# Optimization experiments

Hardware: AMD Instinct MI355X
Metric: run time of the kernel (lower is better)

Reference implementation:

```python
import math
import jax, jax.numpy as jnp
import numpy as np

HEADS = 8
D_MODEL = 256


def positional_encoding_2d(c, h, w):
    # faithful port of wzlxjtu/PositionalEncoding2D
    d = c // 2
    div_term = jnp.exp(jnp.arange(0.0, d, 2, dtype=jnp.float32) * (-(math.log(10000.0) / d)))  # [d//2? no: d/2 entries -> d//2]
    pos_w = jnp.arange(0.0, w, dtype=jnp.float32)[:, None] * div_term  # [w, d//2]
    pos_h = jnp.arange(0.0, h, dtype=jnp.float32)[:, None] * div_term  # [h, d//2]
    pe = jnp.zeros((c, h, w), dtype=jnp.float32)
    sw = jnp.broadcast_to(jnp.sin(pos_w).T[:, None, :], (div_term.shape[0], h, w))
    cw = jnp.broadcast_to(jnp.cos(pos_w).T[:, None, :], (div_term.shape[0], h, w))
    sh = jnp.broadcast_to(jnp.sin(pos_h).T[:, :, None], (div_term.shape[0], h, w))
    ch = jnp.broadcast_to(jnp.cos(pos_h).T[:, :, None], (div_term.shape[0], h, w))
    pe = pe.at[0:d:2].set(sw)
    pe = pe.at[1:d:2].set(cw)
    pe = pe.at[d::2].set(sh)
    pe = pe.at[d + 1::2].set(ch)
    return pe


def setup_inputs() -> dict:
    key = jax.random.key(0)
    ks = jax.random.split(key, 9)
    b, c, h, w = 2, D_MODEL, 64, 64
    x = jax.random.normal(ks[0], (b, c, h, w), dtype=jnp.float32)
    s = 0.02
    Wq = jax.random.normal(ks[1], (c, c), dtype=jnp.float32) * s
    Wk = jax.random.normal(ks[2], (c, c), dtype=jnp.float32) * s
    Wv = jax.random.normal(ks[3], (c, c), dtype=jnp.float32) * s
    Wo = jax.random.normal(ks[4], (c, c), dtype=jnp.float32) * s
    bq = jax.random.normal(ks[5], (c,), dtype=jnp.float32) * s
    bk = jax.random.normal(ks[6], (c,), dtype=jnp.float32) * s
    bv = jax.random.normal(ks[7], (c,), dtype=jnp.float32) * s
    bo = jax.random.normal(ks[8], (c,), dtype=jnp.float32) * s
    return {"x": x, "Wq": Wq, "bq": bq, "Wk": Wk, "bk": bk,
            "Wv": Wv, "bv": bv, "Wo": Wo, "bo": bo}


def reference(x, Wq, bq, Wk, bk, Wv, bv, Wo, bo):
    b, c, h, w = x.shape
    dk = c // HEADS
    pe = positional_encoding_2d(c, h, w)
    x2 = x + pe[None]                                   # [b,c,h,w]
    tok = x2.reshape(b, c, h * w).transpose(0, 2, 1)    # [b,N,c]
    q = (tok @ Wq.T + bq).reshape(b, -1, HEADS, dk).transpose(0, 2, 1, 3)  # [b,H,N,dk]
    k = (tok @ Wk.T + bk).reshape(b, -1, HEADS, dk).transpose(0, 2, 1, 3)
    v = (tok @ Wv.T + bv).reshape(b, -1, HEADS, dk).transpose(0, 2, 1, 3)
    scores = jnp.einsum('bhnd,bhmd->bhnm', q, k) / math.sqrt(dk)  # [b,H,N,N]
    attn = jax.nn.softmax(scores, axis=-1)
    out = jnp.einsum('bhnm,bhmd->bhnd', attn, v)        # [b,H,N,dk]
    concat = out.transpose(0, 2, 1, 3).reshape(b, -1, c)  # [b,N,c]
    proj = concat @ Wo.T + bo                           # [b,N,c]
    return proj.transpose(0, 2, 1).reshape(b, c, h, w)
```

## Files before the change

kernel.cpp:

```cpp
#include <hip/hip_runtime.h>
#include <hip/hip_bf16.h>
#include <cstdint>

typedef float f32x4 __attribute__((ext_vector_type(4)));
typedef __bf16 bf16x8 __attribute__((ext_vector_type(8)));
typedef __bf16 bf16x2 __attribute__((ext_vector_type(2)));
typedef uint32_t uint2v __attribute__((ext_vector_type(2)));

#define MFMA_K32(A, B, C) __builtin_amdgcn_mfma_f32_16x16x32_bf16((A), (B), (C), 0, 0, 0)

#if __has_builtin(__builtin_amdgcn_exp2f)
#define EXP2(x) __builtin_amdgcn_exp2f(x)
#else
#define EXP2(x) exp2f(x)
#endif

static __device__ __forceinline__ uint16_t f2b(float f) {
    uint32_t u = __float_as_uint(f);
    uint32_t r = (u + 0x7fffu + ((u >> 16) & 1u)) >> 16;
    return (uint16_t)r;
}

static __device__ __forceinline__ uint32_t packbf(float a, float b) {
#if __has_builtin(__builtin_amdgcn_cvt_pk_bf16_f32)
    bf16x2 v = __builtin_amdgcn_cvt_pk_bf16_f32(a, b);
    return *(uint32_t*)&v;
#else
    uint32_t ua = __float_as_uint(a);
    ua += 0x7fffu + ((ua >> 16) & 1u);
    uint32_t ub = __float_as_uint(b);
    ub += 0x7fffu + ((ub >> 16) & 1u);
    return __builtin_amdgcn_perm(ub, ua, 0x07060302);
#endif
}

__global__ __launch_bounds__(256) void wconv_pe(const float* __restrict__ wq,
                                                const float* __restrict__ wk,
                                                const float* __restrict__ wv,
                                                const float* __restrict__ wo,
                                                uint16_t* __restrict__ dst,
                                                float* __restrict__ pet) {
    int bid = blockIdx.x, t = threadIdx.x;
    if (bid < 1024) {
        int idx = bid * 256 + t;
        int which = idx >> 16, off = idx & 65535;
        const float* s = (which == 0) ? wq : (which == 1) ? wk : (which == 2) ? wv : wo;
        dst[idx] = f2b(s[off]);
    } else {
        int idx = (bid - 1024) * 256 + t;
        int cc = idx >> 6, p = idx & 63;
        int i = (cc & 127) >> 1;
        float dt = __expf((float)(2 * i) * -0.07195578415606394f);
        float sv, cv;
        __sincosf((float)p * dt, &sv, &cv);
        pet[idx] = (cc & 1) ? cv : sv;
    }
}

__global__ __launch_bounds__(256) void peadd(const float* __restrict__ x,
                                             const float* __restrict__ pet,
                                             uint16_t* __restrict__ tok) {
    __shared__ uint16_t T[64][65];
    int t = threadIdx.x, bid = blockIdx.x;
    int nt = bid & 63, ct = (bid >> 6) & 3, bb = bid >> 8;
    int n0 = nt << 6, c0 = ct << 6;
    int nl = t & 63, cq = t >> 6;
    int n = n0 + nl;
    int posh = n0 >> 6;
#pragma unroll
    for (int p = 0; p < 16; ++p) {
        int cl = cq * 16 + p;
        int cc = c0 + cl;
        float pe = pet[cc * 64 + ((cc & 128) ? posh : nl)];
        T[cl][nl] = f2b(x[((size_t)(bb * 256 + cc) << 12) + n] + pe);
    }
    __syncthreads();
#pragma unroll
    for (int p = 0; p < 16; ++p) {
        int tl = cq * 16 + p;
        tok[(((size_t)(bb << 12) | (n0 + tl)) << 8) + c0 + nl] = T[nl][tl];
    }
}

__global__ __launch_bounds__(256) void qkv_gemm(const uint16_t* __restrict__ tok,
                                                const uint16_t* __restrict__ Wall,
                                                const float* __restrict__ bq,
                                                const float* __restrict__ bk,
                                                const float* __restrict__ bv,
                                                uint16_t* __restrict__ qo,
                                                uint16_t* __restrict__ ko,
                                                uint16_t* __restrict__ vo) {
    __shared__ __align__(16) uint16_t WS[64][264];
    int tid = threadIdx.x, wv = tid >> 6, lane = tid & 63;
    int c16 = lane & 15, quad = lane >> 4;
    int M0 = blockIdx.x * 64 + wv * 16;
    int O0 = blockIdx.y * 64;
    const uint16_t* arow = tok + (size_t)(M0 + c16) * 256;
    bf16x8 af[8];
#pragma unroll
    for (int kk = 0; kk < 8; ++kk) af[kk] = *(const bf16x8*)(arow + kk * 32 + quad * 8);
    f32x4 zero = {0.f, 0.f, 0.f, 0.f};
    int bb = M0 >> 12, n = (M0 + c16) & 4095;
    int srow = tid >> 5, sch = (tid & 31) << 3;
    for (int mat = 0; mat < 3; ++mat) {
        const uint16_t* Wg = Wall + (size_t)mat * 65536 + (size_t)O0 * 256;
        __syncthreads();
#pragma unroll
        for (int p = 0; p < 8; ++p)
            *(bf16x8*)(&WS[p * 8 + srow][sch]) = *(const bf16x8*)(Wg + (p * 8 + srow) * 256 + sch);
        __syncthreads();
        f32x4 acc[4] = {zero, zero, zero, zero};
#pragma unroll
        for (int kk = 0; kk < 8; ++kk) {
            int k0 = kk * 32 + quad * 8;
#pragma unroll
            for (int nb = 0; nb < 4; ++nb)
                acc[nb] = MFMA_K32(*(const bf16x8*)(&WS[nb * 16 + c16][k0]),
                                   af[kk], acc[nb]);
        }
        const float* bias = (mat == 0) ? bq : (mat == 1) ? bk : bv;
        if (mat < 2) {
            float scale = (mat == 0) ? 0.25505654134660127f : 1.0f;
            uint16_t* dst = (mat == 0) ? qo : ko;
#pragma unroll
            for (int nb = 0; nb < 4; ++nb) {
                int o = O0 + nb * 16 + quad * 4;
                f32x4 bi = *(const f32x4*)(bias + o);
                int h = o >> 5, dd = o & 31;
                uint2v pk;
                pk[0] = packbf((acc[nb][0] + bi[0]) * scale, (acc[nb][1] + bi[1]) * scale);
                pk[1] = packbf((acc[nb][2] + bi[2]) * scale, (acc[nb][3] + bi[3]) * scale);
                *(uint2v*)(dst + ((size_t)(bb * 8 + h) * 4096 + n) * 32 + dd) = pk;
            }
        } else {
#pragma unroll
            for (int nb = 0; nb < 4; ++nb)
#pragma unroll
                for (int r = 0; r < 4; ++r) {
                    int o = O0 + nb * 16 + quad * 4 + r;
                    vo[((size_t)(bb * 8 + (o >> 5)) * 32 + (o & 31)) * 4096 + n] =
                        f2b(acc[nb][r] + bias[o]);
                }
        }
    }
}

static __device__ __forceinline__ void attn_qblock(const bf16x8 (&kf)[4],
                                                   const bf16x8 (&vA)[2],
                                                   const bf16x8 (&vB)[2],
                                                   bf16x8 ones, bf16x8 qf,
                                                   f32x4& oA, f32x4& oB, f32x4& oS) {
    f32x4 zero = {0.f, 0.f, 0.f, 0.f};
    f32x4 s[4];
#pragma unroll
    for (int c = 0; c < 4; ++c) s[c] = MFMA_K32(kf[c], qf, zero);
#pragma unroll
    for (int p = 0; p < 2; ++p) {
#pragma unroll
        for (int r = 0; r < 4; ++r) {
            s[2 * p][r] = EXP2(s[2 * p][r]);
            s[2 * p + 1][r] = EXP2(s[2 * p + 1][r]);
        }
        union { bf16x8 v; uint32_t u[4]; } pa;
        pa.u[0] = packbf(s[2 * p][0], s[2 * p][1]);
        pa.u[1] = packbf(s[2 * p][2], s[2 * p][3]);
        pa.u[2] = packbf(s[2 * p + 1][0], s[2 * p + 1][1]);
        pa.u[3] = packbf(s[2 * p + 1][2], s[2 * p + 1][3]);
        oA = MFMA_K32(pa.v, vA[p], oA);
        oB = MFMA_K32(pa.v, vB[p], oB);
        oS = MFMA_K32(pa.v, ones, oS);
    }
}

__global__ __launch_bounds__(512, 4) void flash(const uint16_t* __restrict__ qb,
                                                const uint16_t* __restrict__ kb,
                                                const uint16_t* __restrict__ vtb,
                                                uint16_t* __restrict__ concat) {
    __shared__ __align__(16) char smem[43008];
    int tid = threadIdx.x, wv = tid >> 6, lane = tid & 63;
    int c16 = lane & 15, quad = lane >> 4;
    int half = tid >> 8, t2 = tid & 255;
    int bh = blockIdx.y;
    int q0 = (blockIdx.x << 7) + (wv & 3) * 32;
    size_t base = (size_t)bh << 12;

    uint16_t* KT = (uint16_t*)(smem + half * 21504);
    uint16_t* VT = (uint16_t*)(smem + half * 21504 + 12288);

    const uint16_t* kgp = kb + (base + (size_t)half * 2048 + (t2 >> 2)) * 32 + (t2 & 3) * 8;
    const uint16_t* vgp = vtb + ((size_t)bh * 32 + (t2 >> 3)) * 4096 + half * 2048 + (t2 & 7) * 8;
    uint16_t* kls = KT + (t2 >> 2) * 48 + (t2 & 3) * 8;
    uint16_t* vls = VT + (t2 >> 3) * 72 + (t2 & 7) * 8;

    bf16x8 qf0 = *(const bf16x8*)(qb + (base + q0 + c16) * 32 + quad * 8);
    bf16x8 qf1 = *(const bf16x8*)(qb + (base + q0 + 16 + c16) * 32 + quad * 8);

    int rbase = ((c16 >> 2) << 3) + (c16 & 3);

    union { uint32_t u[4]; bf16x8 v; } onesu;
    onesu.u[0] = 0x3F803F80u; onesu.u[1] = 0x3F803F80u;
    onesu.u[2] = 0x3F803F80u; onesu.u[3] = 0x3F803F80u;
    bf16x8 ones = onesu.v;

    f32x4 zero = {0.f, 0.f, 0.f, 0.f};
    f32x4 o00 = zero, o01 = zero, o10 = zero, o11 = zero;
    f32x4 oS0 = zero, oS1 = zero;

    {
        bf16x8 kr = *(const bf16x8*)kgp;
        bf16x8 vr = *(const bf16x8*)vgp;
        *(bf16x8*)kls = kr;
        *(bf16x8*)vls = vr;
    }
    __syncthreads();

    for (int kt = 0; kt < 32; ++kt) {
        int cur = kt & 1;
        int kn = (kt + 1) & 31;
        bf16x8 kr = *(const bf16x8*)(kgp + (size_t)kn * 2048);
        bf16x8 vr = *(const bf16x8*)(vgp + kn * 64);
        const uint16_t* kfp = KT + cur * 3072 + rbase * 48 + quad * 8;
        const uint16_t* vfp = VT + cur * 2304 + c16 * 72 + quad * 8;
        bf16x8 kf[4], vA[2], vB[2];
        kf[0] = *(const bf16x8*)(kfp);
        kf[1] = *(const bf16x8*)(kfp + 192);
        kf[2] = *(const bf16x8*)(kfp + 1536);
        kf[3] = *(const bf16x8*)(kfp + 1536 + 192);
        vA[0] = *(const bf16x8*)(vfp);
        vA[1] = *(const bf16x8*)(vfp + 32);
        vB[0] = *(const bf16x8*)(vfp + 1152);
        vB[1] = *(const bf16x8*)(vfp + 1152 + 32);
        attn_qblock(kf, vA, vB, ones, qf0, o00, o01, oS0);
        attn_qblock(kf, vA, vB, ones, qf1, o10, o11, oS1);
        *(bf16x8*)(kls + (cur ^ 1) * 3072) = kr;
        *(bf16x8*)(vls + (cur ^ 1) * 2304) = vr;
        __syncthreads();
    }

    float* ov = (float*)smem;
    if (wv >= 4) {
        float* d = ov + ((wv - 4) * 64 + lane) * 25;
#pragma unroll
        for (int r = 0; r < 4; ++r) {
            d[r] = o00[r]; d[4 + r] = o01[r]; d[8 + r] = o10[r]; d[12 + r] = o11[r];
            d[16 + r] = oS0[r]; d[20 + r] = oS1[r];
        }
    }
    __syncthreads();
    if (wv < 4) {
        const float* s = ov + (wv * 64 + lane) * 25;
#pragma unroll
        for (int r = 0; r < 4; ++r) {
            o00[r] += s[r]; o01[r] += s[4 + r]; o10[r] += s[8 + r]; o11[r] += s[12 + r];
            oS0[r] += s[16 + r]; oS1[r] += s[20 + r];
        }
        int h = bh & 7, bb = bh >> 3;
#pragma unroll
        for (int r = 0; r < 4; ++r) {
            float i0 = 1.f / oS0[r];
            float i1 = 1.f / oS1[r];
            int n = q0 + quad * 4 + r;
            size_t row0 = ((size_t)bb * 4096 + n) * 256 + h * 32;
            size_t row1 = ((size_t)bb * 4096 + n + 16) * 256 + h * 32;
            concat[row0 + c16]      = f2b(o00[r] * i0);
            concat[row0 + 16 + c16] = f2b(o01[r] * i0);
            concat[row1 + c16]      = f2b(o10[r] * i1);
            concat[row1 + 16 + c16] = f2b(o11[r] * i1);
        }
    }
}

__global__ __launch_bounds__(256) void proj_gemm(const uint16_t* __restrict__ concat,
                                                 const uint16_t* __restrict__ Wo,
                                                 const float* __restrict__ bo,
                                                 float* __restrict__ out) {
    __shared__ __align__(16) uint16_t WS[64][264];
    int tid = threadIdx.x, wv = tid >> 6, lane = tid & 63;
    int c16 = lane & 15, quad = lane >> 4;
    int M0 = blockIdx.x * 64 + wv * 16;
    int O0 = blockIdx.y * 64;
    int srow = tid >> 5, sch = (tid & 31) << 3;
    const uint16_t* Wg = Wo + (size_t)O0 * 256;
#pragma unroll
    for (int p = 0; p < 8; ++p)
        *(bf16x8*)(&WS[p * 8 + srow][sch]) = *(const bf16x8*)(Wg + (p * 8 + srow) * 256 + sch);
    const uint16_t* crow = concat + (size_t)(M0 + c16) * 256;
    bf16x8 af[8];
#pragma unroll
    for (int kk = 0; kk < 8; ++kk) af[kk] = *(const bf16x8*)(crow + kk * 32 + quad * 8);
    __syncthreads();
    f32x4 zero = {0.f, 0.f, 0.f, 0.f};
    f32x4 acc[4] = {zero, zero, zero, zero};
#pragma unroll
    for (int kk = 0; kk < 8; ++kk) {
        int k0 = kk * 32 + quad * 8;
#pragma unroll
        for (int nb = 0; nb < 4; ++nb)
            acc[nb] = MFMA_K32(*(const bf16x8*)(&WS[nb * 16 + c16][k0]),
                               af[kk], acc[nb]);
    }
    int bb = M0 >> 12, n = (M0 + c16) & 4095;
#pragma unroll
    for (int nb = 0; nb < 4; ++nb)
#pragma unroll
        for (int r = 0; r < 4; ++r) {
            int o = O0 + nb * 16 + quad * 4 + r;
            out[((size_t)(bb * 256 + o) << 12) + n] = acc[nb][r] + bo[o];
        }
}

extern "C" void kernel_launch(void* const* d_in, const int* in_sizes, int n_in,
                              void* d_out, int out_size, void* d_ws, size_t ws_size,
                              hipStream_t stream) {
    const float* x  = (const float*)d_in[0];
    const float* Wq = (const float*)d_in[1];
    const float* bq = (const float*)d_in[2];
    const float* Wk = (const float*)d_in[3];
    const float* bk = (const float*)d_in[4];
    const float* Wv = (const float*)d_in[5];
    const float* bv = (const float*)d_in[6];
    const float* Wo = (const float*)d_in[7];
    const float* bo = (const float*)d_in[8];
    float* out = (float*)d_out;

    uint16_t* ws   = (uint16_t*)d_ws;
    uint16_t* Wb   = ws;
    uint16_t* tok  = Wb + 4 * 65536;
    uint16_t* q    = tok + 2097152;
    uint16_t* k    = q + 2097152;
    uint16_t* vt   = k + 2097152;
    uint16_t* cc   = vt + 2097152;
    float*    pet  = (float*)(cc + 2097152);

    wconv_pe<<<1088, 256, 0, stream>>>(Wq, Wk, Wv, Wo, Wb, pet);
    peadd<<<512, 256, 0, stream>>>(x, pet, tok);
    qkv_gemm<<<dim3(128, 4), 256, 0, stream>>>(tok, Wb, bq, bk, bv, q, k, vt);
    flash<<<dim3(32, 16), 512, 0, stream>>>(q, k, vt, cc);
    proj_gemm<<<dim3(128, 4), 256, 0, stream>>>(cc, Wb + 3 * 65536, bo, out);
}
```

Before: 150.3 us.

## Fuse weight conversion and PE into consumers, shrink K smem padding, interleave attention blocks

Removes the separate weight-conversion and positional-encoding kernel. Weights are now converted from fp32 to bf16 while being staged into shared memory inside the QKV and projection GEMMs, and the positional encoding is computed inline in peadd with sincos. In the flash kernel the K tile row stride drops from 48 to 40, which reduces shared memory per block. The two query sub-block computations are also interleaved so their MFMA and exp chains can overlap. The cost is that each GEMM block re-reads and re-converts fp32 weights, and peadd redoes transcendental math per element.

```diff
diff --git a/kernel.cpp b/kernel.cpp
--- a/kernel.cpp
+++ b/kernel.cpp
@@ -6,6 +6,7 @@
 typedef __bf16 bf16x8 __attribute__((ext_vector_type(8)));
 typedef __bf16 bf16x2 __attribute__((ext_vector_type(2)));
 typedef uint32_t uint2v __attribute__((ext_vector_type(2)));
+typedef uint32_t uint4v __attribute__((ext_vector_type(4)));
 
 #define MFMA_K32(A, B, C) __builtin_amdgcn_mfma_f32_16x16x32_bf16((A), (B), (C), 0, 0, 0)
 
@@ -34,31 +35,7 @@
 #endif
 }
 
-__global__ __launch_bounds__(256) void wconv_pe(const float* __restrict__ wq,
-                                                const float* __restrict__ wk,
-                                                const float* __restrict__ wv,
-                                                const float* __restrict__ wo,
-                                                uint16_t* __restrict__ dst,
-                                                float* __restrict__ pet) {
-    int bid = blockIdx.x, t = threadIdx.x;
-    if (bid < 1024) {
-        int idx = bid * 256 + t;
-        int which = idx >> 16, off = idx & 65535;
-        const float* s = (which == 0) ? wq : (which == 1) ? wk : (which == 2) ? wv : wo;
-        dst[idx] = f2b(s[off]);
-    } else {
-        int idx = (bid - 1024) * 256 + t;
-        int cc = idx >> 6, p = idx & 63;
-        int i = (cc & 127) >> 1;
-        float dt = __expf((float)(2 * i) * -0.07195578415606394f);
-        float sv, cv;
-        __sincosf((float)p * dt, &sv, &cv);
-        pet[idx] = (cc & 1) ? cv : sv;
-    }
-}
-
 __global__ __launch_bounds__(256) void peadd(const float* __restrict__ x,
-                                             const float* __restrict__ pet,
                                              uint16_t* __restrict__ tok) {
     __shared__ uint16_t T[64][65];
     int t = threadIdx.x, bid = blockIdx.x;
@@ -67,11 +44,16 @@
     int nl = t & 63, cq = t >> 6;
     int n = n0 + nl;
     int posh = n0 >> 6;
+    float pf = (float)((c0 & 128) ? posh : nl);
 #pragma unroll
     for (int p = 0; p < 16; ++p) {
         int cl = cq * 16 + p;
         int cc = c0 + cl;
-        float pe = pet[cc * 64 + ((cc & 128) ? posh : nl)];
+        int i = (cc & 127) >> 1;
+        float dt = __expf((float)(2 * i) * -0.07195578415606394f);
+        float sv, cv;
+        __sincosf(pf * dt, &sv, &cv);
+        float pe = (cc & 1) ? cv : sv;
         T[cl][nl] = f2b(x[((size_t)(bb * 256 + cc) << 12) + n] + pe);
     }
     __syncthreads();
@@ -83,7 +65,9 @@
 }
 
 __global__ __launch_bounds__(256) void qkv_gemm(const uint16_t* __restrict__ tok,
-                                                const uint16_t* __restrict__ Wall,
+                                                const float* __restrict__ wqp,
+                                                const float* __restrict__ wkp,
+                                                const float* __restrict__ wvp,
                                                 const float* __restrict__ bq,
                                                 const float* __restrict__ bk,
                                                 const float* __restrict__ bv,
@@ -103,11 +87,20 @@
     int bb = M0 >> 12, n = (M0 + c16) & 4095;
     int srow = tid >> 5, sch = (tid & 31) << 3;
     for (int mat = 0; mat < 3; ++mat) {
-        const uint16_t* Wg = Wall + (size_t)mat * 65536 + (size_t)O0 * 256;
+        const float* Wg = ((mat == 0) ? wqp : (mat == 1) ? wkp : wvp) + (size_t)O0 * 256;
         __syncthreads();
 #pragma unroll
-        for (int p = 0; p < 8; ++p)
-            *(bf16x8*)(&WS[p * 8 + srow][sch]) = *(const bf16x8*)(Wg + (p * 8 + srow) * 256 + sch);
+        for (int p = 0; p < 8; ++p) {
+            const float* src = Wg + (size_t)(p * 8 + srow) * 256 + sch;
+            f32x4 lo = *(const f32x4*)(src);
+            f32x4 hi = *(const f32x4*)(src + 4);
+            uint4v pk;
+            pk[0] = packbf(lo[0], lo[1]);
+            pk[1] = packbf(lo[2], lo[3]);
+            pk[2] = packbf(hi[0], hi[1]);
+            pk[3] = packbf(hi[2], hi[3]);
+            *(uint4v*)(&WS[p * 8 + srow][sch]) = pk;
+        }
         __syncthreads();
         f32x4 acc[4] = {zero, zero, zero, zero};
 #pragma unroll
@@ -145,38 +138,11 @@
     }
 }
 
-static __device__ __forceinline__ void attn_qblock(const bf16x8 (&kf)[4],
-                                                   const bf16x8 (&vA)[2],
-                                                   const bf16x8 (&vB)[2],
-                                                   bf16x8 ones, bf16x8 qf,
-                                                   f32x4& oA, f32x4& oB, f32x4& oS) {
-    f32x4 zero = {0.f, 0.f, 0.f, 0.f};
-    f32x4 s[4];
-#pragma unroll
-    for (int c = 0; c < 4; ++c) s[c] = MFMA_K32(kf[c], qf, zero);
-#pragma unroll
-    for (int p = 0; p < 2; ++p) {
-#pragma unroll
-        for (int r = 0; r < 4; ++r) {
-            s[2 * p][r] = EXP2(s[2 * p][r]);
-            s[2 * p + 1][r] = EXP2(s[2 * p + 1][r]);
-        }
-        union { bf16x8 v; uint32_t u[4]; } pa;
-        pa.u[0] = packbf(s[2 * p][0], s[2 * p][1]);
-        pa.u[1] = packbf(s[2 * p][2], s[2 * p][3]);
-        pa.u[2] = packbf(s[2 * p + 1][0], s[2 * p + 1][1]);
-        pa.u[3] = packbf(s[2 * p + 1][2], s[2 * p + 1][3]);
-        oA = MFMA_K32(pa.v, vA[p], oA);
-        oB = MFMA_K32(pa.v, vB[p], oB);
-        oS = MFMA_K32(pa.v, ones, oS);
-    }
-}
-
 __global__ __launch_bounds__(512, 4) void flash(const uint16_t* __restrict__ qb,
                                                 const uint16_t* __restrict__ kb,
                                                 const uint16_t* __restrict__ vtb,
                                                 uint16_t* __restrict__ concat) {
-    __shared__ __align__(16) char smem[43008];
+    __shared__ __align__(16) char smem[38912];
     int tid = threadIdx.x, wv = tid >> 6, lane = tid & 63;
     int c16 = lane & 15, quad = lane >> 4;
     int half = tid >> 8, t2 = tid & 255;
@@ -184,12 +150,12 @@
     int q0 = (blockIdx.x << 7) + (wv & 3) * 32;
     size_t base = (size_t)bh << 12;
 
-    uint16_t* KT = (uint16_t*)(smem + half * 21504);
-    uint16_t* VT = (uint16_t*)(smem + half * 21504 + 12288);
+    uint16_t* KT = (uint16_t*)(smem + half * 19456);
+    uint16_t* VT = (uint16_t*)(smem + half * 19456 + 10240);
 
     const uint16_t* kgp = kb + (base + (size_t)half * 2048 + (t2 >> 2)) * 32 + (t2 & 3) * 8;
     const uint16_t* vgp = vtb + ((size_t)bh * 32 + (t2 >> 3)) * 4096 + half * 2048 + (t2 & 7) * 8;
-    uint16_t* kls = KT + (t2 >> 2) * 48 + (t2 & 3) * 8;
+    uint16_t* kls = KT + (t2 >> 2) * 40 + (t2 & 3) * 8;
     uint16_t* vls = VT + (t2 >> 3) * 72 + (t2 & 7) * 8;
 
     bf16x8 qf0 = *(const bf16x8*)(qb + (base + q0 + c16) * 32 + quad * 8);
@@ -219,20 +185,51 @@
         int kn = (kt + 1) & 31;
         bf16x8 kr = *(const bf16x8*)(kgp + (size_t)kn * 2048);
         bf16x8 vr = *(const bf16x8*)(vgp + kn * 64);
-        const uint16_t* kfp = KT + cur * 3072 + rbase * 48 + quad * 8;
+        const uint16_t* kfp = KT + cur * 2560 + rbase * 40 + quad * 8;
         const uint16_t* vfp = VT + cur * 2304 + c16 * 72 + quad * 8;
         bf16x8 kf[4], vA[2], vB[2];
         kf[0] = *(const bf16x8*)(kfp);
-        kf[1] = *(const bf16x8*)(kfp + 192);
-        kf[2] = *(const bf16x8*)(kfp + 1536);
-        kf[3] = *(const bf16x8*)(kfp + 1536 + 192);
+        kf[1] = *(const bf16x8*)(kfp + 160);
+        kf[2] = *(const bf16x8*)(kfp + 1280);
+        kf[3] = *(const bf16x8*)(kfp + 1440);
         vA[0] = *(const bf16x8*)(vfp);
         vA[1] = *(const bf16x8*)(vfp + 32);
         vB[0] = *(const bf16x8*)(vfp + 1152);
         vB[1] = *(const bf16x8*)(vfp + 1152 + 32);
-        attn_qblock(kf, vA, vB, ones, qf0, o00, o01, oS0);
-        attn_qblock(kf, vA, vB, ones, qf1, o10, o11, oS1);
-        *(bf16x8*)(kls + (cur ^ 1) * 3072) = kr;
+
+        f32x4 s0[4], s1[4];
+#pragma unroll
+        for (int c = 0; c < 4; ++c) s0[c] = MFMA_K32(kf[c], qf0, zero);
+#pragma unroll
+        for (int c = 0; c < 4; ++c) s1[c] = MFMA_K32(kf[c], qf1, zero);
+
+#pragma unroll
+        for (int p = 0; p < 2; ++p) {
+#pragma unroll
+            for (int r = 0; r < 4; ++r) {
+                s0[2 * p][r] = EXP2(s0[2 * p][r]);
+                s0[2 * p + 1][r] = EXP2(s0[2 * p + 1][r]);
+                s1[2 * p][r] = EXP2(s1[2 * p][r]);
+                s1[2 * p + 1][r] = EXP2(s1[2 * p + 1][r]);
+            }
+            union { bf16x8 v; uint32_t u[4]; } pa0, pa1;
+            pa0.u[0] = packbf(s0[2 * p][0], s0[2 * p][1]);
+            pa0.u[1] = packbf(s0[2 * p][2], s0[2 * p][3]);
+            pa0.u[2] = packbf(s0[2 * p + 1][0], s0[2 * p + 1][1]);
+            pa0.u[3] = packbf(s0[2 * p + 1][2], s0[2 * p + 1][3]);
+            pa1.u[0] = packbf(s1[2 * p][0], s1[2 * p][1]);
+            pa1.u[1] = packbf(s1[2 * p][2], s1[2 * p][3]);
+            pa1.u[2] = packbf(s1[2 * p + 1][0], s1[2 * p + 1][1]);
+            pa1.u[3] = packbf(s1[2 * p + 1][2], s1[2 * p + 1][3]);
+            o00 = MFMA_K32(pa0.v, vA[p], o00);
+            o01 = MFMA_K32(pa0.v, vB[p], o01);
+            oS0 = MFMA_K32(pa0.v, ones, oS0);
+            o10 = MFMA_K32(pa1.v, vA[p], o10);
+            o11 = MFMA_K32(pa1.v, vB[p], o11);
+            oS1 = MFMA_K32(pa1.v, ones, oS1);
+        }
+
+        *(bf16x8*)(kls + (cur ^ 1) * 2560) = kr;
         *(bf16x8*)(vls + (cur ^ 1) * 2304) = vr;
         __syncthreads();
     }
@@ -271,7 +268,7 @@
 }
 
 __global__ __launch_bounds__(256) void proj_gemm(const uint16_t* __restrict__ concat,
-                                                 const uint16_t* __restrict__ Wo,
+                                                 const float* __restrict__ Wo,
                                                  const float* __restrict__ bo,
                                                  float* __restrict__ out) {
     __shared__ __align__(16) uint16_t WS[64][264];
@@ -280,10 +277,19 @@
     int M0 = blockIdx.x * 64 + wv * 16;
     int O0 = blockIdx.y * 64;
     int srow = tid >> 5, sch = (tid & 31) << 3;
-    const uint16_t* Wg = Wo + (size_t)O0 * 256;
-#pragma unroll
-    for (int p = 0; p < 8; ++p)
-        *(bf16x8*)(&WS[p * 8 + srow][sch]) = *(const bf16x8*)(Wg + (p * 8 + srow) * 256 + sch);
+    const float* Wg = Wo + (size_t)O0 * 256;
+#pragma unroll
+    for (int p = 0; p < 8; ++p) {
+        const float* src = Wg + (size_t)(p * 8 + srow) * 256 + sch;
+        f32x4 lo = *(const f32x4*)(src);
+        f32x4 hi = *(const f32x4*)(src + 4);
+        uint4v pk;
+        pk[0] = packbf(lo[0], lo[1]);
+        pk[1] = packbf(lo[2], lo[3]);
+        pk[2] = packbf(hi[0], hi[1]);
+        pk[3] = packbf(hi[2], hi[3]);
+        *(uint4v*)(&WS[p * 8 + srow][sch]) = pk;
+    }
     const uint16_t* crow = concat + (size_t)(M0 + c16) * 256;
     bf16x8 af[8];
 #pragma unroll
@@ -324,17 +330,14 @@
     float* out = (float*)d_out;
 
     uint16_t* ws   = (uint16_t*)d_ws;
-    uint16_t* Wb   = ws;
-    uint16_t* tok  = Wb + 4 * 65536;
+    uint16_t* tok  = ws;
     uint16_t* q    = tok + 2097152;
     uint16_t* k    = q + 2097152;
     uint16_t* vt   = k + 2097152;
     uint16_t* cc   = vt + 2097152;
-    float*    pet  = (float*)(cc + 2097152);
-
-    wconv_pe<<<1088, 256, 0, stream>>>(Wq, Wk, Wv, Wo, Wb, pet);
-    peadd<<<512, 256, 0, stream>>>(x, pet, tok);
-    qkv_gemm<<<dim3(128, 4), 256, 0, stream>>>(tok, Wb, bq, bk, bv, q, k, vt);
+
+    peadd<<<512, 256, 0, stream>>>(x, tok);
+    qkv_gemm<<<dim3(128, 4), 256, 0, stream>>>(tok, Wq, Wk, Wv, bq, bk, bv, q, k, vt);
     flash<<<dim3(32, 16), 512, 0, stream>>>(q, k, vt, cc);
-    proj_gemm<<<dim3(128, 4), 256, 0, stream>>>(cc, Wb + 3 * 65536, bo, out);
-}
+    proj_gemm<<<dim3(128, 4), 256, 0, stream>>>(cc, Wo, bo, out);
+}
```

Result: slower. 154.9 us (+3.1%).

## Interleave two query blocks' MFMA/exp chains, shrink K LDS padding, force pk_bf16 asm

Applied to the files above, without the earlier changes.

The per-query-block helper is inlined, and the QK MFMAs, exp2, packing and PV MFMAs for both 32-row query blocks are interleaved so independent work can hide MFMA and transcendental latency. The K tile row pitch in shared memory drops from 48 to 40 elements, which reduces LDS use and changes the bank-conflict pattern. bf16 packing is forced to the v_cvt_pk_bf16_f32 instruction via inline asm. Interleaving raises register pressure under launch_bounds(512,4), and the new padding may add bank conflicts.

```diff
diff --git a/kernel.cpp b/kernel.cpp
--- a/kernel.cpp
+++ b/kernel.cpp
@@ -4,7 +4,6 @@
 
 typedef float f32x4 __attribute__((ext_vector_type(4)));
 typedef __bf16 bf16x8 __attribute__((ext_vector_type(8)));
-typedef __bf16 bf16x2 __attribute__((ext_vector_type(2)));
 typedef uint32_t uint2v __attribute__((ext_vector_type(2)));
 
 #define MFMA_K32(A, B, C) __builtin_amdgcn_mfma_f32_16x16x32_bf16((A), (B), (C), 0, 0, 0)
@@ -22,16 +21,9 @@
 }
 
 static __device__ __forceinline__ uint32_t packbf(float a, float b) {
-#if __has_builtin(__builtin_amdgcn_cvt_pk_bf16_f32)
-    bf16x2 v = __builtin_amdgcn_cvt_pk_bf16_f32(a, b);
-    return *(uint32_t*)&v;
-#else
-    uint32_t ua = __float_as_uint(a);
-    ua += 0x7fffu + ((ua >> 16) & 1u);
-    uint32_t ub = __float_as_uint(b);
-    ub += 0x7fffu + ((ub >> 16) & 1u);
-    return __builtin_amdgcn_perm(ub, ua, 0x07060302);
-#endif
+    uint32_t r;
+    asm("v_cvt_pk_bf16_f32 %0, %1, %2" : "=v"(r) : "v"(a), "v"(b));
+    return r;
 }
 
 __global__ __launch_bounds__(256) void wconv_pe(const float* __restrict__ wq,
@@ -145,38 +137,11 @@
     }
 }
 
-static __device__ __forceinline__ void attn_qblock(const bf16x8 (&kf)[4],
-                                                   const bf16x8 (&vA)[2],
-                                                   const bf16x8 (&vB)[2],
-                                                   bf16x8 ones, bf16x8 qf,
-                                                   f32x4& oA, f32x4& oB, f32x4& oS) {
-    f32x4 zero = {0.f, 0.f, 0.f, 0.f};
-    f32x4 s[4];
-#pragma unroll
-    for (int c = 0; c < 4; ++c) s[c] = MFMA_K32(kf[c], qf, zero);
-#pragma unroll
-    for (int p = 0; p < 2; ++p) {
-#pragma unroll
-        for (int r = 0; r < 4; ++r) {
-            s[2 * p][r] = EXP2(s[2 * p][r]);
-            s[2 * p + 1][r] = EXP2(s[2 * p + 1][r]);
-        }
-        union { bf16x8 v; uint32_t u[4]; } pa;
-        pa.u[0] = packbf(s[2 * p][0], s[2 * p][1]);
-        pa.u[1] = packbf(s[2 * p][2], s[2 * p][3]);
-        pa.u[2] = packbf(s[2 * p + 1][0], s[2 * p + 1][1]);
-        pa.u[3] = packbf(s[2 * p + 1][2], s[2 * p + 1][3]);
-        oA = MFMA_K32(pa.v, vA[p], oA);
-        oB = MFMA_K32(pa.v, vB[p], oB);
-        oS = MFMA_K32(pa.v, ones, oS);
-    }
-}
-
 __global__ __launch_bounds__(512, 4) void flash(const uint16_t* __restrict__ qb,
                                                 const uint16_t* __restrict__ kb,
                                                 const uint16_t* __restrict__ vtb,
                                                 uint16_t* __restrict__ concat) {
-    __shared__ __align__(16) char smem[43008];
+    __shared__ __align__(16) char smem[38912];
     int tid = threadIdx.x, wv = tid >> 6, lane = tid & 63;
     int c16 = lane & 15, quad = lane >> 4;
     int half = tid >> 8, t2 = tid & 255;
@@ -184,12 +149,12 @@
     int q0 = (blockIdx.x << 7) + (wv & 3) * 32;
     size_t base = (size_t)bh << 12;
 
-    uint16_t* KT = (uint16_t*)(smem + half * 21504);
-    uint16_t* VT = (uint16_t*)(smem + half * 21504 + 12288);
+    uint16_t* KT = (uint16_t*)(smem + half * 19456);
+    uint16_t* VT = (uint16_t*)(smem + half * 19456 + 10240);
 
     const uint16_t* kgp = kb + (base + (size_t)half * 2048 + (t2 >> 2)) * 32 + (t2 & 3) * 8;
     const uint16_t* vgp = vtb + ((size_t)bh * 32 + (t2 >> 3)) * 4096 + half * 2048 + (t2 & 7) * 8;
-    uint16_t* kls = KT + (t2 >> 2) * 48 + (t2 & 3) * 8;
+    uint16_t* kls = KT + (t2 >> 2) * 40 + (t2 & 3) * 8;
     uint16_t* vls = VT + (t2 >> 3) * 72 + (t2 & 7) * 8;
 
     bf16x8 qf0 = *(const bf16x8*)(qb + (base + q0 + c16) * 32 + quad * 8);
@@ -219,20 +184,51 @@
         int kn = (kt + 1) & 31;
         bf16x8 kr = *(const bf16x8*)(kgp + (size_t)kn * 2048);
         bf16x8 vr = *(const bf16x8*)(vgp + kn * 64);
-        const uint16_t* kfp = KT + cur * 3072 + rbase * 48 + quad * 8;
+        const uint16_t* kfp = KT + cur * 2560 + rbase * 40 + quad * 8;
         const uint16_t* vfp = VT + cur * 2304 + c16 * 72 + quad * 8;
         bf16x8 kf[4], vA[2], vB[2];
         kf[0] = *(const bf16x8*)(kfp);
-        kf[1] = *(const bf16x8*)(kfp + 192);
-        kf[2] = *(const bf16x8*)(kfp + 1536);
-        kf[3] = *(const bf16x8*)(kfp + 1536 + 192);
+        kf[1] = *(const bf16x8*)(kfp + 160);
+        kf[2] = *(const bf16x8*)(kfp + 1280);
+        kf[3] = *(const bf16x8*)(kfp + 1440);
         vA[0] = *(const bf16x8*)(vfp);
         vA[1] = *(const bf16x8*)(vfp + 32);
         vB[0] = *(const bf16x8*)(vfp + 1152);
         vB[1] = *(const bf16x8*)(vfp + 1152 + 32);
-        attn_qblock(kf, vA, vB, ones, qf0, o00, o01, oS0);
-        attn_qblock(kf, vA, vB, ones, qf1, o10, o11, oS1);
-        *(bf16x8*)(kls + (cur ^ 1) * 3072) = kr;
+
+        f32x4 s0[4], s1[4];
+#pragma unroll
+        for (int c = 0; c < 4; ++c) s0[c] = MFMA_K32(kf[c], qf0, zero);
+#pragma unroll
+        for (int c = 0; c < 4; ++c) s1[c] = MFMA_K32(kf[c], qf1, zero);
+
+#pragma unroll
+        for (int p = 0; p < 2; ++p) {
+#pragma unroll
+            for (int r = 0; r < 4; ++r) {
+                s0[2 * p][r] = EXP2(s0[2 * p][r]);
+                s0[2 * p + 1][r] = EXP2(s0[2 * p + 1][r]);
+                s1[2 * p][r] = EXP2(s1[2 * p][r]);
+                s1[2 * p + 1][r] = EXP2(s1[2 * p + 1][r]);
+            }
+            union { bf16x8 v; uint32_t u[4]; } pa0, pa1;
+            pa0.u[0] = packbf(s0[2 * p][0], s0[2 * p][1]);
+            pa0.u[1] = packbf(s0[2 * p][2], s0[2 * p][3]);
+            pa0.u[2] = packbf(s0[2 * p + 1][0], s0[2 * p + 1][1]);
+            pa0.u[3] = packbf(s0[2 * p + 1][2], s0[2 * p + 1][3]);
+            pa1.u[0] = packbf(s1[2 * p][0], s1[2 * p][1]);
+            pa1.u[1] = packbf(s1[2 * p][2], s1[2 * p][3]);
+            pa1.u[2] = packbf(s1[2 * p + 1][0], s1[2 * p + 1][1]);
+            pa1.u[3] = packbf(s1[2 * p + 1][2], s1[2 * p + 1][3]);
+            o00 = MFMA_K32(pa0.v, vA[p], o00);
+            o01 = MFMA_K32(pa0.v, vB[p], o01);
+            oS0 = MFMA_K32(pa0.v, ones, oS0);
+            o10 = MFMA_K32(pa1.v, vA[p], o10);
+            o11 = MFMA_K32(pa1.v, vB[p], o11);
+            oS1 = MFMA_K32(pa1.v, ones, oS1);
+        }
+
+        *(bf16x8*)(kls + (cur ^ 1) * 2560) = kr;
         *(bf16x8*)(vls + (cur ^ 1) * 2304) = vr;
         __syncthreads();
     }
```

Result: faster. 134.6 us (-10.4%).
